# Kernel tuning notes

Measured on AMD Instinct MI355X. Metric: run time of the kernel, lower is better.

The kernel has to match this reference:

```python
import jax, jax.numpy as jnp
import numpy as np

H = 16          # num_heads
EPS = 1e-6      # RMSNorm eps


def setup_inputs() -> dict:
    key = jax.random.key(0)
    ks = jax.random.split(key, 5)
    B, N, D = 4, 4096, 1024
    x = jax.random.normal(ks[0], (B, N, D), dtype=jnp.float32)
    q = jax.random.normal(ks[1], (D,), dtype=jnp.float32)
    k = jax.random.normal(ks[2], (D,), dtype=jnp.float32)
    log_decay = jax.random.normal(ks[3], (H,), dtype=jnp.float32)
    norm_weight = jnp.ones((D,), dtype=jnp.float32)
    o_w = jax.random.normal(ks[4], (D, D), dtype=jnp.float32) * 0.02
    return {"x": x, "q": q, "k": k, "log_decay": log_decay,
            "norm_weight": norm_weight, "o_w": o_w}


def reference(x, q, k, log_decay, norm_weight, o_w):
    b, n, dm = x.shape
    dh = dm // H
    qh = q.reshape(H, dh)            # per-head query vector (constant over b, n)
    kh = k.reshape(H, dh)            # per-head key vector
    v = x.reshape(b, n, H, dh)       # values = input tokens
    # exp(logsigmoid(a)) == sigmoid(a): per-head decay in (0, 1)
    lam = jax.nn.sigmoid(log_decay)  # (H,)

    def step(S, v_t):
        # S: (b, H, dh, dh) recurrent state;  v_t: (b, H, dh)
        S = lam[None, :, None, None] * S + kh[None, :, :, None] * v_t[:, :, None, :]
        o_t = jnp.einsum('hd,bhdv->bhv', qh, S)
        return S, o_t

    S0 = jnp.zeros((b, H, dh, dh), dtype=x.dtype)
    _, o = jax.lax.scan(step, S0, jnp.moveaxis(v, 1, 0))  # o: (n, b, H, dh)
    o = jnp.moveaxis(o, 0, 1).reshape(b, n, dm)

    # RMSNorm over the channel dim
    o = o * jax.lax.rsqrt(jnp.mean(o * o, axis=-1, keepdims=True) + EPS) * norm_weight
    # o_proj (no bias)
    return o @ o_w.T
```

## Files before the change

kernel.cpp:

```cpp
#include <hip/hip_runtime.h>
#include <hip/hip_bf16.h>
#include <cstdint>
#include <cstddef>

#define HH   16
#define BB   4
#define NN   4096
#define DD   1024
#define MM   (BB * NN)
#define NC   128
#define LC   32
#define EPSV 1e-6f

typedef short short8 __attribute__((ext_vector_type(8)));
typedef float floatx4 __attribute__((ext_vector_type(4)));

__device__ __forceinline__ void async_copy16(const void* g, void* l) {
    __builtin_amdgcn_global_load_lds(
        (const __attribute__((address_space(1))) void*)g,
        (__attribute__((address_space(3))) void*)l, 16, 0, 0);
}

__global__ void k_meta(const float* __restrict__ q, const float* __restrict__ k,
                       const float* __restrict__ ld, float* __restrict__ meta) {
    int tid = threadIdx.x;
    float p = q[tid] * k[tid];
    #pragma unroll
    for (int off = 32; off > 0; off >>= 1) p += __shfl_xor(p, off);
    if ((tid & 63) == 0) meta[16 + (tid >> 6)] = p;
    if (tid < HH) meta[tid] = 1.f / (1.f + expf(-ld[tid]));
}

__global__ void k_wconv(const float* __restrict__ ow, const float* __restrict__ nw,
                        __hip_bfloat16* __restrict__ wp) {
    size_t i = (size_t)blockIdx.x * 256 + threadIdx.x;
    int j = (int)(i & (DD - 1));
    wp[i] = __float2bfloat16(ow[i] * nw[j]);
}

__global__ void k_chunk_end(const float* __restrict__ x, const float* __restrict__ meta,
                            float* __restrict__ E) {
    int b = blockIdx.x / NC, c = blockIdx.x % NC;
    int j = threadIdx.x;
    float lam = meta[j >> 6];
    const float* xp = x + ((size_t)(b * NN + c * LC)) * DD + j;
    float e = 0.f;
    #pragma unroll
    for (int t = 0; t < LC; ++t) e = fmaf(lam, e, xp[(size_t)t * DD]);
    E[(size_t)blockIdx.x * DD + j] = e;
}

__global__ void k_carry(const float* __restrict__ meta, const float* __restrict__ E,
                        float* __restrict__ P) {
    int g = blockIdx.x * 256 + threadIdx.x;
    int b = g >> 10, j = g & 1023;
    float lam = meta[j >> 6];
    float lamL = lam;
    lamL *= lamL; lamL *= lamL; lamL *= lamL; lamL *= lamL; lamL *= lamL;
    float p = 0.f;
    for (int c = 0; c < NC; ++c) {
        size_t idx = ((size_t)(b * NC + c)) * DD + j;
        P[idx] = p;
        p = fmaf(lamL, p, E[idx]);
    }
}

__global__ void k_scan(const float* __restrict__ x, const float* __restrict__ meta,
                       const float* __restrict__ P, __hip_bfloat16* __restrict__ obf,
                       float* __restrict__ sumsq) {
    __shared__ float wpart[16];
    int b = blockIdx.x / NC, c = blockIdx.x % NC;
    int j = threadIdx.x;
    int h = j >> 6;
    float lam = meta[h];
    float ch  = meta[16 + h];
    int row0 = b * NN + c * LC;
    const float* xp = x + (size_t)row0 * DD + j;
    float y = P[(size_t)blockIdx.x * DD + j];
    for (int t = 0; t < LC; ++t) {
        y = fmaf(lam, y, xp[(size_t)t * DD]);
        float o = ch * y;
        obf[(size_t)(row0 + t) * DD + j] = __float2bfloat16(o);
        float s = o * o;
        #pragma unroll
        for (int off = 32; off > 0; off >>= 1) s += __shfl_xor(s, off);
        if ((j & 63) == 0) wpart[h] = s;
        __syncthreads();
        if (j == 0) {
            float tot = 0.f;
            #pragma unroll
            for (int wv = 0; wv < 16; ++wv) tot += wpart[wv];
            sumsq[row0 + t] = tot;
        }
        __syncthreads();
    }
}

__launch_bounds__(256)
__global__ void k_gemm(const __hip_bfloat16* __restrict__ A,
                       const __hip_bfloat16* __restrict__ W,
                       const float* __restrict__ sumsq, float* __restrict__ out) {
    __shared__ __attribute__((aligned(16))) short sA[128 * 32];
    __shared__ __attribute__((aligned(16))) short sB[128 * 32];
    const int tid = threadIdx.x;
    const int l = tid & 63, w = tid >> 6;
    const int wm = w >> 1, wn = w & 1;
    const int bm = blockIdx.x >> 3, bn = blockIdx.x & 7;
    const int m0 = bm * 128, n0 = bn * 128;
    const short* Ag = (const short*)A;
    const short* Wg = (const short*)W;

    floatx4 acc[4][4] = {};
    const int srow = w * 16 + (l >> 2);
    const int scol = (l & 3) * 8;

    for (int kt = 0; kt < 32; ++kt) {
        const int k0 = kt * 32;
        #pragma unroll
        for (int i = 0; i < 2; ++i) {
            async_copy16(Ag + (size_t)(m0 + i * 64 + srow) * 1024 + k0 + scol,
                         (char*)sA + i * 4096 + w * 1024);
            async_copy16(Wg + (size_t)(n0 + i * 64 + srow) * 1024 + k0 + scol,
                         (char*)sB + i * 4096 + w * 1024);
        }
        __syncthreads();
        short8 af[4], bf[4];
        #pragma unroll
        for (int mt = 0; mt < 4; ++mt)
            af[mt] = *(const short8*)(sA + (wm * 64 + mt * 16 + (l & 15)) * 32 + (l >> 4) * 8);
        #pragma unroll
        for (int nt = 0; nt < 4; ++nt)
            bf[nt] = *(const short8*)(sB + (wn * 64 + nt * 16 + (l & 15)) * 32 + (l >> 4) * 8);
        #pragma unroll
        for (int mt = 0; mt < 4; ++mt)
            #pragma unroll
            for (int nt = 0; nt < 4; ++nt)
                acc[mt][nt] = __builtin_amdgcn_mfma_f32_16x16x32_bf16(af[mt], bf[nt], acc[mt][nt], 0, 0, 0);
        __syncthreads();
    }

    #pragma unroll
    for (int mt = 0; mt < 4; ++mt) {
        #pragma unroll
        for (int r = 0; r < 4; ++r) {
            int mrow = m0 + wm * 64 + mt * 16 + (l >> 4) * 4 + r;
            float rs = rsqrtf(sumsq[mrow] * (1.f / 1024.f) + EPSV);
            #pragma unroll
            for (int nt = 0; nt < 4; ++nt) {
                int col = n0 + wn * 64 + nt * 16 + (l & 15);
                out[(size_t)mrow * 1024 + col] = acc[mt][nt][r] * rs;
            }
        }
    }
}

extern "C" void kernel_launch(void* const* d_in, const int* in_sizes, int n_in,
                              void* d_out, int out_size, void* d_ws, size_t ws_size,
                              hipStream_t stream) {
    const float* x  = (const float*)d_in[0];
    const float* q  = (const float*)d_in[1];
    const float* k  = (const float*)d_in[2];
    const float* ld = (const float*)d_in[3];
    const float* nw = (const float*)d_in[4];
    const float* ow = (const float*)d_in[5];
    float* out = (float*)d_out;

    char* ws = (char*)d_ws;
    float* meta  = (float*)(ws + 0);
    float* sumsq = (float*)(ws + 256);
    float* E     = (float*)(ws + 65792);
    float* P     = (float*)(ws + 2162944);
    __hip_bfloat16* Wp  = (__hip_bfloat16*)(ws + 4260096);
    __hip_bfloat16* Obf = (__hip_bfloat16*)(ws + 6357248);

    k_meta<<<1, 1024, 0, stream>>>(q, k, ld, meta);
    k_wconv<<<(DD * DD) / 256, 256, 0, stream>>>(ow, nw, Wp);
    k_chunk_end<<<BB * NC, 1024, 0, stream>>>(x, meta, E);
    k_carry<<<16, 256, 0, stream>>>(meta, E, P);
    k_scan<<<BB * NC, 1024, 0, stream>>>(x, meta, P, Obf, sumsq);
    k_gemm<<<(MM / 128) * (DD / 128), 256, 0, stream>>>(Obf, Wp, sumsq, out);
}
```

Baseline: 217.7 us.

## Parallelize carry scan, atomic sumsq, and widen GEMM K-tile with swizzled LDS

The carry kernel moves from 16 blocks each running a serial 128-step loop to one block per (batch, channel) chain that runs a Hillis-Steele parallel scan in shared memory. The per-step block-wide reduction and the two barriers in k_scan are replaced by per-wave atomicAdd into sumsq, which is now zeroed by a memset. The GEMM K-tile grows from 32 to 64 with an XOR-swizzled LDS layout to avoid bank conflicts, and its block order is changed so consecutive blocks share the same weight tile. These changes cut serialization and barrier stalls, at the cost of extra launches, atomics and a float summation order that is no longer fixed.

After: 199.9 us. 8.2% less time.

```diff
diff --git a/kernel.cpp b/kernel.cpp
--- a/kernel.cpp
+++ b/kernel.cpp
@@ -40,7 +40,7 @@
 
 __global__ void k_chunk_end(const float* __restrict__ x, const float* __restrict__ meta,
                             float* __restrict__ E) {
-    int b = blockIdx.x / NC, c = blockIdx.x % NC;
+    int b = blockIdx.x >> 7, c = blockIdx.x & (NC - 1);
     int j = threadIdx.x;
     float lam = meta[j >> 6];
     const float* xp = x + ((size_t)(b * NN + c * LC)) * DD + j;
@@ -52,24 +52,34 @@
 
 __global__ void k_carry(const float* __restrict__ meta, const float* __restrict__ E,
                         float* __restrict__ P) {
-    int g = blockIdx.x * 256 + threadIdx.x;
-    int b = g >> 10, j = g & 1023;
+    __shared__ float sa[NC], sb[NC];
+    int chain = blockIdx.x;
+    int b = chain >> 10, j = chain & 1023;
+    int c = threadIdx.x;
     float lam = meta[j >> 6];
     float lamL = lam;
     lamL *= lamL; lamL *= lamL; lamL *= lamL; lamL *= lamL; lamL *= lamL;
-    float p = 0.f;
-    for (int c = 0; c < NC; ++c) {
-        size_t idx = ((size_t)(b * NC + c)) * DD + j;
-        P[idx] = p;
-        p = fmaf(lamL, p, E[idx]);
-    }
+    size_t idx = ((size_t)(b * NC + c)) * DD + j;
+    float a = lamL, bv = E[idx];
+    sa[c] = a; sb[c] = bv;
+    #pragma unroll
+    for (int d = 1; d < NC; d <<= 1) {
+        __syncthreads();
+        float pa = 1.f, pb = 0.f;
+        if (c >= d) { pa = sa[c - d]; pb = sb[c - d]; }
+        __syncthreads();
+        bv = fmaf(a, pb, bv);
+        a  = a * pa;
+        sa[c] = a; sb[c] = bv;
+    }
+    __syncthreads();
+    P[idx] = (c == 0) ? 0.f : sb[c - 1];
 }
 
 __global__ void k_scan(const float* __restrict__ x, const float* __restrict__ meta,
                        const float* __restrict__ P, __hip_bfloat16* __restrict__ obf,
                        float* __restrict__ sumsq) {
-    __shared__ float wpart[16];
-    int b = blockIdx.x / NC, c = blockIdx.x % NC;
+    int b = blockIdx.x >> 7, c = blockIdx.x & (NC - 1);
     int j = threadIdx.x;
     int h = j >> 6;
     float lam = meta[h];
@@ -84,15 +94,7 @@
         float s = o * o;
         #pragma unroll
         for (int off = 32; off > 0; off >>= 1) s += __shfl_xor(s, off);
-        if ((j & 63) == 0) wpart[h] = s;
-        __syncthreads();
-        if (j == 0) {
-            float tot = 0.f;
-            #pragma unroll
-            for (int wv = 0; wv < 16; ++wv) tot += wpart[wv];
-            sumsq[row0 + t] = tot;
-        }
-        __syncthreads();
+        if ((j & 63) == 0) atomicAdd(&sumsq[row0 + t], s);
     }
 }
 
@@ -100,42 +102,58 @@
 __global__ void k_gemm(const __hip_bfloat16* __restrict__ A,
                        const __hip_bfloat16* __restrict__ W,
                        const float* __restrict__ sumsq, float* __restrict__ out) {
-    __shared__ __attribute__((aligned(16))) short sA[128 * 32];
-    __shared__ __attribute__((aligned(16))) short sB[128 * 32];
+    __shared__ __attribute__((aligned(16))) short sA[128 * 64];
+    __shared__ __attribute__((aligned(16))) short sB[128 * 64];
     const int tid = threadIdx.x;
     const int l = tid & 63, w = tid >> 6;
     const int wm = w >> 1, wn = w & 1;
-    const int bm = blockIdx.x >> 3, bn = blockIdx.x & 7;
+    const int g = blockIdx.x;
+    const int bm = g & 127, bn = g >> 7;
     const int m0 = bm * 128, n0 = bn * 128;
     const short* Ag = (const short*)A;
     const short* Wg = (const short*)W;
 
     floatx4 acc[4][4] = {};
-    const int srow = w * 16 + (l >> 2);
-    const int scol = (l & 3) * 8;
-
-    for (int kt = 0; kt < 32; ++kt) {
-        const int k0 = kt * 32;
-        #pragma unroll
-        for (int i = 0; i < 2; ++i) {
-            async_copy16(Ag + (size_t)(m0 + i * 64 + srow) * 1024 + k0 + scol,
+
+    int srow[4], scol[4];
+    #pragma unroll
+    for (int i = 0; i < 4; ++i) {
+        int s = i * 256 + tid;
+        srow[i] = s >> 3;
+        scol[i] = ((s & 7) ^ ((s >> 3) & 7)) * 8;
+    }
+
+    for (int kt = 0; kt < 16; ++kt) {
+        const int k0 = kt * 64;
+        #pragma unroll
+        for (int i = 0; i < 4; ++i) {
+            async_copy16(Ag + (size_t)(m0 + srow[i]) * 1024 + k0 + scol[i],
                          (char*)sA + i * 4096 + w * 1024);
-            async_copy16(Wg + (size_t)(n0 + i * 64 + srow) * 1024 + k0 + scol,
+            async_copy16(Wg + (size_t)(n0 + srow[i]) * 1024 + k0 + scol[i],
                          (char*)sB + i * 4096 + w * 1024);
         }
         __syncthreads();
-        short8 af[4], bf[4];
-        #pragma unroll
-        for (int mt = 0; mt < 4; ++mt)
-            af[mt] = *(const short8*)(sA + (wm * 64 + mt * 16 + (l & 15)) * 32 + (l >> 4) * 8);
-        #pragma unroll
-        for (int nt = 0; nt < 4; ++nt)
-            bf[nt] = *(const short8*)(sB + (wn * 64 + nt * 16 + (l & 15)) * 32 + (l >> 4) * 8);
-        #pragma unroll
-        for (int mt = 0; mt < 4; ++mt)
-            #pragma unroll
-            for (int nt = 0; nt < 4; ++nt)
-                acc[mt][nt] = __builtin_amdgcn_mfma_f32_16x16x32_bf16(af[mt], bf[nt], acc[mt][nt], 0, 0, 0);
+        #pragma unroll
+        for (int ks = 0; ks < 2; ++ks) {
+            short8 af[4], bf[4];
+            #pragma unroll
+            for (int mt = 0; mt < 4; ++mt) {
+                int row = wm * 64 + mt * 16 + (l & 15);
+                int c8  = (ks * 4 + (l >> 4)) ^ (row & 7);
+                af[mt] = *(const short8*)(sA + row * 64 + c8 * 8);
+            }
+            #pragma unroll
+            for (int nt = 0; nt < 4; ++nt) {
+                int row = wn * 64 + nt * 16 + (l & 15);
+                int c8  = (ks * 4 + (l >> 4)) ^ (row & 7);
+                bf[nt] = *(const short8*)(sB + row * 64 + c8 * 8);
+            }
+            #pragma unroll
+            for (int mt = 0; mt < 4; ++mt)
+                #pragma unroll
+                for (int nt = 0; nt < 4; ++nt)
+                    acc[mt][nt] = __builtin_amdgcn_mfma_f32_16x16x32_bf16(af[mt], bf[nt], acc[mt][nt], 0, 0, 0);
+        }
         __syncthreads();
     }
 
@@ -173,10 +191,11 @@
     __hip_bfloat16* Wp  = (__hip_bfloat16*)(ws + 4260096);
     __hip_bfloat16* Obf = (__hip_bfloat16*)(ws + 6357248);
 
+    hipMemsetAsync(sumsq, 0, MM * sizeof(float), stream);
     k_meta<<<1, 1024, 0, stream>>>(q, k, ld, meta);
     k_wconv<<<(DD * DD) / 256, 256, 0, stream>>>(ow, nw, Wp);
     k_chunk_end<<<BB * NC, 1024, 0, stream>>>(x, meta, E);
-    k_carry<<<16, 256, 0, stream>>>(meta, E, P);
+    k_carry<<<BB * DD, NC, 0, stream>>>(meta, E, P);
     k_scan<<<BB * NC, 1024, 0, stream>>>(x, meta, P, Obf, sumsq);
     k_gemm<<<(MM / 128) * (DD / 128), 256, 0, stream>>>(Obf, Wp, sumsq, out);
 }
```
